# Performance work log

Measured on AMD Instinct MI355X. Metric: run time of the kernel, lower is better.

## Reference

```python
import jax, jax.numpy as jnp
import numpy as np

D_MODEL = 1024
NUM_HEADS = 16
D_K = D_MODEL // NUM_HEADS
SCALE = D_K ** 0.5


def setup_inputs() -> dict:
    key = jax.random.key(0)
    ks = jax.random.split(key, 11)
    B, S = 2, 2048
    std = 1.0 / np.sqrt(D_MODEL)
    inp = {
        "query": jax.random.normal(ks[0], (B, S, D_MODEL), dtype=jnp.float32),
        "key": jax.random.normal(ks[1], (B, S, D_MODEL), dtype=jnp.float32),
        "value": jax.random.normal(ks[2], (B, S, D_MODEL), dtype=jnp.float32),
        "wq": jax.random.uniform(ks[3], (D_MODEL, D_MODEL), jnp.float32, -std, std),
        "bq": jax.random.uniform(ks[4], (D_MODEL,), jnp.float32, -std, std),
        "wk": jax.random.uniform(ks[5], (D_MODEL, D_MODEL), jnp.float32, -std, std),
        "bk": jax.random.uniform(ks[6], (D_MODEL,), jnp.float32, -std, std),
        "wv": jax.random.uniform(ks[7], (D_MODEL, D_MODEL), jnp.float32, -std, std),
        "bv": jax.random.uniform(ks[8], (D_MODEL,), jnp.float32, -std, std),
        "wo": jax.random.uniform(ks[9], (D_MODEL, D_MODEL), jnp.float32, -std, std),
        "bo": jax.random.uniform(ks[10], (D_MODEL,), jnp.float32, -std, std),
    }
    return inp


def _split_heads(x):
    # [B, S, d_model] -> [B, H, S, d_k]
    B, S, _ = x.shape
    return x.reshape(B, S, NUM_HEADS, D_K).transpose(0, 2, 1, 3)


def reference(query, key, value, wq, bq, wk, bk, wv, bv, wo, bo):
    # Linear layers: torch Linear computes x @ W^T + b; weights here stored as [out, in]
    q = _split_heads(query @ wq.T + bq)  # [B, H, S, d_k]
    k = _split_heads(key @ wk.T + bk)
    v = _split_heads(value @ wv.T + bv)
    scores = jnp.einsum("bhqd,bhkd->bhqk", q, k) / SCALE  # [B, H, Sq, Sk]
    attn = jax.nn.softmax(scores, axis=-1)
    ctx = jnp.einsum("bhqk,bhkd->bhqd", attn, v)  # [B, H, S, d_k]
    B, H, S, dk = ctx.shape
    ctx = ctx.transpose(0, 2, 1, 3).reshape(B, S, D_MODEL)
    return ctx @ wo.T + bo
```

## Files before the change

kernel.cpp:

```cpp
#include <hip/hip_runtime.h>
#include <hip/hip_bf16.h>


typedef __attribute__((ext_vector_type(8))) short short8;
typedef __attribute__((ext_vector_type(4))) float floatx4;

#define D_MODEL 1024
#define SEQ 2048
#define NTOK 4096
#define DK 64
#define NH 16
#define MAT 4194304
#define WMAT 1048576

static __device__ __forceinline__ unsigned short f2bf(float f) {
    unsigned int x = __float_as_uint(f);
    unsigned int r = x + 0x7fffu + ((x >> 16) & 1u);
    return (unsigned short)(r >> 16);
}
static __device__ __forceinline__ float bf2f(unsigned short u) {
    return __uint_as_float(((unsigned int)u) << 16);
}
static __device__ __forceinline__ unsigned pk2(float x, float y) {
    __hip_bfloat162 h = __float22bfloat162_rn(make_float2(x, y));
    return *reinterpret_cast<unsigned*>(&h);
}
static __device__ __forceinline__ short8 cvt8(float4 f0, float4 f1) {
    union { unsigned u[4]; short8 s; } r;
    r.u[0] = pk2(f0.x, f0.y); r.u[1] = pk2(f0.z, f0.w);
    r.u[2] = pk2(f1.x, f1.y); r.u[3] = pk2(f1.z, f1.w);
    return r.s;
}

__global__ __launch_bounds__(256) void cvt7(
    const float* __restrict__ s0, const float* __restrict__ s1,
    const float* __restrict__ s2, const float* __restrict__ s3,
    const float* __restrict__ s4, const float* __restrict__ s5,
    const float* __restrict__ s6, unsigned short* __restrict__ dst) {
    const float* s; size_t doff; int n;
    switch (blockIdx.y) {
        case 0: s = s0; doff = 0;                          n = MAT;  break;
        case 1: s = s1; doff = (size_t)MAT;                n = MAT;  break;
        case 2: s = s2; doff = (size_t)2 * MAT;            n = MAT;  break;
        case 3: s = s3; doff = (size_t)3 * MAT;            n = WMAT; break;
        case 4: s = s4; doff = (size_t)3 * MAT + WMAT;     n = WMAT; break;
        case 5: s = s5; doff = (size_t)3 * MAT + 2 * WMAT; n = WMAT; break;
        default: s = s6; doff = (size_t)3 * MAT + 3 * WMAT; n = WMAT; break;
    }
    int idx = (blockIdx.x * 256 + threadIdx.x) * 8;
    if (idx >= n) return;
    float4 a = *(const float4*)(s + idx);
    float4 b = *(const float4*)(s + idx + 4);
    *(short8*)&dst[doff + idx] = cvt8(a, b);
}

template <bool F32OUT, bool ROWBIAS, int OSTRIDE>
static __device__ __forceinline__ void gemm_bb(const unsigned short* __restrict__ X,
                                               const unsigned short* __restrict__ W,
                                               const float* __restrict__ bias,
                                               void* __restrict__ outp) {
    __shared__ __align__(16) unsigned short Asm[128 * 72];
    __shared__ __align__(16) unsigned short Bsm[128 * 72];

    const int tid = threadIdx.x;
    const int lane = tid & 63;
    const int wv = tid >> 6;
    const int g = lane >> 4;
    const int lm = lane & 15;
    const int wr = wv >> 1;
    const int wc = wv & 1;
    const int m0 = blockIdx.y * 128;
    const int n0 = blockIdx.x * 128;

    floatx4 acc[4][4];
#pragma unroll
    for (int mi = 0; mi < 4; ++mi)
#pragma unroll
        for (int ni = 0; ni < 4; ++ni)
            acc[mi][ni] = (floatx4){0.f, 0.f, 0.f, 0.f};

    for (int k0 = 0; k0 < 1024; k0 += 64) {
#pragma unroll
        for (int i = 0; i < 4; ++i) {
            int idx = tid + i * 256;
            int row = idx >> 3;
            int col = (idx & 7) << 3;
            *(uint4*)&Asm[row * 72 + col] =
                *(const uint4*)&X[(size_t)(m0 + row) * 1024 + k0 + col];
            *(uint4*)&Bsm[row * 72 + col] =
                *(const uint4*)&W[(size_t)(n0 + row) * 1024 + k0 + col];
        }
        __syncthreads();
#pragma unroll
        for (int ks = 0; ks < 64; ks += 32) {
            short8 af[4], bfr[4];
#pragma unroll
            for (int mi = 0; mi < 4; ++mi)
                af[mi] = *(const short8*)&Asm[(wr * 64 + mi * 16 + lm) * 72 + ks + g * 8];
#pragma unroll
            for (int ni = 0; ni < 4; ++ni)
                bfr[ni] = *(const short8*)&Bsm[(wc * 64 + ni * 16 + lm) * 72 + ks + g * 8];
#pragma unroll
            for (int mi = 0; mi < 4; ++mi)
#pragma unroll
                for (int ni = 0; ni < 4; ++ni)
                    acc[mi][ni] = __builtin_amdgcn_mfma_f32_16x16x32_bf16(
                        af[mi], bfr[ni], acc[mi][ni], 0, 0, 0);
        }
        __syncthreads();
    }

    float cb[4];
#pragma unroll
    for (int ni = 0; ni < 4; ++ni)
        cb[ni] = ROWBIAS ? 0.f : bias[n0 + wc * 64 + ni * 16 + lm];
#pragma unroll
    for (int mi = 0; mi < 4; ++mi)
#pragma unroll
        for (int r = 0; r < 4; ++r) {
            int rowg = m0 + wr * 64 + mi * 16 + g * 4 + r;
            float rb = ROWBIAS ? bias[rowg] : 0.f;
#pragma unroll
            for (int ni = 0; ni < 4; ++ni) {
                int colg = n0 + wc * 64 + ni * 16 + lm;
                float val = acc[mi][ni][r] + (ROWBIAS ? rb : cb[ni]);
                if (F32OUT)
                    ((float*)outp)[(size_t)rowg * OSTRIDE + colg] = val;
                else
                    ((unsigned short*)outp)[(size_t)rowg * OSTRIDE + colg] = f2bf(val);
            }
        }
}

__global__ __launch_bounds__(256) void qkv_gemm_b(
    const unsigned short* __restrict__ Xb, const unsigned short* __restrict__ Wb,
    const float* __restrict__ bq, const float* __restrict__ bk,
    unsigned short* __restrict__ QK) {
    const int z = blockIdx.z;
    const float* bias = (z == 0) ? bq : bk;
    gemm_bb<false, false, 1024>(Xb + (size_t)z * MAT, Wb + (size_t)z * WMAT, bias,
                                QK + (size_t)z * MAT);
}

__global__ __launch_bounds__(256) void vt_gemm_b(
    const unsigned short* __restrict__ Wv, const unsigned short* __restrict__ Xv,
    const float* __restrict__ bv, unsigned short* __restrict__ VT) {
    gemm_bb<false, true, 4096>(Wv, Xv, bv, VT);
}

__global__ __launch_bounds__(256) void out_gemm_b(
    const unsigned short* __restrict__ ctx, const unsigned short* __restrict__ Wo,
    const float* __restrict__ bo, float* __restrict__ out) {
    gemm_bb<true, false, 1024>(ctx, Wo, bo, out);
}

template <bool ROWBIAS, int OSTRIDE>
static __device__ __forceinline__ void gemm128_f(const float* __restrict__ X,
                                                 const float* __restrict__ W,
                                                 const float* __restrict__ bias,
                                                 unsigned short* __restrict__ out) {
    __shared__ __align__(16) unsigned short Asm[128 * 72];
    __shared__ __align__(16) unsigned short Bsm[128 * 72];
    const int tid = threadIdx.x;
    const int lane = tid & 63;
    const int wv = tid >> 6;
    const int g = lane >> 4;
    const int lm = lane & 15;
    const int wr = wv >> 1;
    const int wc = wv & 1;
    const int m0 = blockIdx.y * 128;
    const int n0 = blockIdx.x * 128;
    floatx4 acc[4][4];
#pragma unroll
    for (int mi = 0; mi < 4; ++mi)
#pragma unroll
        for (int ni = 0; ni < 4; ++ni)
            acc[mi][ni] = (floatx4){0.f, 0.f, 0.f, 0.f};
    for (int k0 = 0; k0 < 1024; k0 += 64) {
#pragma unroll
        for (int i = 0; i < 4; ++i) {
            int idx = tid + i * 256;
            int row = idx >> 3;
            int col = (idx & 7) << 3;
            const float* sa = &X[(size_t)(m0 + row) * 1024 + k0 + col];
            *(short8*)&Asm[row * 72 + col] = cvt8(*(const float4*)sa, *(const float4*)(sa + 4));
            const float* sb = &W[(size_t)(n0 + row) * 1024 + k0 + col];
            *(short8*)&Bsm[row * 72 + col] = cvt8(*(const float4*)sb, *(const float4*)(sb + 4));
        }
        __syncthreads();
#pragma unroll
        for (int ks = 0; ks < 64; ks += 32) {
            short8 af[4], bfr[4];
#pragma unroll
            for (int mi = 0; mi < 4; ++mi)
                af[mi] = *(const short8*)&Asm[(wr * 64 + mi * 16 + lm) * 72 + ks + g * 8];
#pragma unroll
            for (int ni = 0; ni < 4; ++ni)
                bfr[ni] = *(const short8*)&Bsm[(wc * 64 + ni * 16 + lm) * 72 + ks + g * 8];
#pragma unroll
            for (int mi = 0; mi < 4; ++mi)
#pragma unroll
                for (int ni = 0; ni < 4; ++ni)
                    acc[mi][ni] = __builtin_amdgcn_mfma_f32_16x16x32_bf16(
                        af[mi], bfr[ni], acc[mi][ni], 0, 0, 0);
        }
        __syncthreads();
    }
    float cb[4];
#pragma unroll
    for (int ni = 0; ni < 4; ++ni)
        cb[ni] = ROWBIAS ? 0.f : bias[n0 + wc * 64 + ni * 16 + lm];
#pragma unroll
    for (int mi = 0; mi < 4; ++mi)
#pragma unroll
        for (int r = 0; r < 4; ++r) {
            int rowg = m0 + wr * 64 + mi * 16 + g * 4 + r;
            float rb = ROWBIAS ? bias[rowg] : 0.f;
#pragma unroll
            for (int ni = 0; ni < 4; ++ni) {
                int colg = n0 + wc * 64 + ni * 16 + lm;
                out[(size_t)rowg * OSTRIDE + colg] =
                    f2bf(acc[mi][ni][r] + (ROWBIAS ? rb : cb[ni]));
            }
        }
}

__global__ __launch_bounds__(256) void qkv_gemm_f(
    const float* __restrict__ xq, const float* __restrict__ xk,
    const float* __restrict__ wq, const float* __restrict__ wk,
    const float* __restrict__ bq, const float* __restrict__ bk,
    unsigned short* __restrict__ q, unsigned short* __restrict__ k) {
    if (blockIdx.z == 0) gemm128_f<false, 1024>(xq, wq, bq, q);
    else                 gemm128_f<false, 1024>(xk, wk, bk, k);
}

__global__ __launch_bounds__(256) void vt_gemm_f(
    const float* __restrict__ wv, const float* __restrict__ xv,
    const float* __restrict__ bv, unsigned short* __restrict__ VT) {
    gemm128_f<true, 4096>(wv, xv, bv, VT);
}

__global__ __launch_bounds__(256) void out_gemm_f(
    const float* __restrict__ wo, const float* __restrict__ bo,
    const unsigned short* __restrict__ ctx, float* __restrict__ out) {
    __shared__ __align__(16) unsigned short Asm[128 * 72];
    __shared__ __align__(16) unsigned short Bsm[128 * 72];
    const int tid = threadIdx.x;
    const int lane = tid & 63;
    const int wv = tid >> 6;
    const int g = lane >> 4;
    const int lm = lane & 15;
    const int wr = wv >> 1;
    const int wc = wv & 1;
    const int m0 = blockIdx.y * 128;
    const int n0 = blockIdx.x * 128;
    floatx4 acc[4][4];
#pragma unroll
    for (int mi = 0; mi < 4; ++mi)
#pragma unroll
        for (int ni = 0; ni < 4; ++ni)
            acc[mi][ni] = (floatx4){0.f, 0.f, 0.f, 0.f};
    for (int k0 = 0; k0 < 1024; k0 += 64) {
#pragma unroll
        for (int i = 0; i < 4; ++i) {
            int idx = tid + i * 256;
            int row = idx >> 3;
            int col = (idx & 7) << 3;
            *(uint4*)&Asm[row * 72 + col] =
                *(const uint4*)&ctx[(size_t)(m0 + row) * 1024 + k0 + col];
            const float* sb = &wo[(size_t)(n0 + row) * 1024 + k0 + col];
            *(short8*)&Bsm[row * 72 + col] = cvt8(*(const float4*)sb, *(const float4*)(sb + 4));
        }
        __syncthreads();
#pragma unroll
        for (int ks = 0; ks < 64; ks += 32) {
            short8 af[4], bfr[4];
#pragma unroll
            for (int mi = 0; mi < 4; ++mi)
                af[mi] = *(const short8*)&Asm[(wr * 64 + mi * 16 + lm) * 72 + ks + g * 8];
#pragma unroll
            for (int ni = 0; ni < 4; ++ni)
                bfr[ni] = *(const short8*)&Bsm[(wc * 64 + ni * 16 + lm) * 72 + ks + g * 8];
#pragma unroll
            for (int mi = 0; mi < 4; ++mi)
#pragma unroll
                for (int ni = 0; ni < 4; ++ni)
                    acc[mi][ni] = __builtin_amdgcn_mfma_f32_16x16x32_bf16(
                        af[mi], bfr[ni], acc[mi][ni], 0, 0, 0);
        }
        __syncthreads();
    }
    float bb[4];
#pragma unroll
    for (int ni = 0; ni < 4; ++ni)
        bb[ni] = bo[n0 + wc * 64 + ni * 16 + lm];
#pragma unroll
    for (int mi = 0; mi < 4; ++mi)
#pragma unroll
        for (int ni = 0; ni < 4; ++ni)
#pragma unroll
            for (int r = 0; r < 4; ++r) {
                int rowg = m0 + wr * 64 + mi * 16 + g * 4 + r;
                int colg = n0 + wc * 64 + ni * 16 + lm;
                out[(size_t)rowg * 1024 + colg] = acc[mi][ni][r] + bb[ni];
            }
}

__global__ __launch_bounds__(256) void attn_kernel(
    const unsigned short* __restrict__ Q, const unsigned short* __restrict__ K,
    const unsigned short* __restrict__ VT, unsigned short* __restrict__ CTX) {
    __shared__ __align__(16) unsigned short Ksm[64 * 72];
    __shared__ __align__(16) unsigned short Vt[64 * 72];

    const int tid = threadIdx.x;
    const int lane = tid & 63;
    const int w = tid >> 6;
    const int g = lane >> 4;
    const int lm = lane & 15;
    const int qt = blockIdx.x;
    const int bh = blockIdx.y;
    const int b = bh >> 4;
    const int h = bh & 15;

    const size_t base = (size_t)b * SEQ * D_MODEL + (size_t)h * DK;
    const size_t vtbase = (size_t)(h * 64) * NTOK + (size_t)b * SEQ;

    const int srow0 = tid >> 3;
    const int scol = (tid & 7) << 3;

    short8 qf[2];
    const int qrow = qt * 64 + w * 16 + lm;
#pragma unroll
    for (int t = 0; t < 2; ++t) {
        short8 raw = *(const short8*)&Q[base + (size_t)qrow * D_MODEL + t * 32 + g * 8];
        union { unsigned u[4]; short8 s; } r;
#pragma unroll
        for (int j = 0; j < 4; ++j) {
            float lo = bf2f((unsigned short)raw[2 * j]) * 0.125f;
            float hi = bf2f((unsigned short)raw[2 * j + 1]) * 0.125f;
            r.u[j] = pk2(lo, hi);
        }
        qf[t] = r.s;
    }

    float lsum = 0.f;
    floatx4 Oacc[4];
#pragma unroll
    for (int nb = 0; nb < 4; ++nb) Oacc[nb] = (floatx4){0.f, 0.f, 0.f, 0.f};

    for (int kt = 0; kt < SEQ / 64; ++kt) {
        const int krow0 = kt * 64;
#pragma unroll
        for (int i = 0; i < 2; ++i) {
            int row = srow0 + i * 32;
            *(uint4*)&Ksm[row * 72 + scol] =
                *(const uint4*)&K[base + (size_t)(krow0 + row) * D_MODEL + scol];
            *(uint4*)&Vt[row * 72 + scol] =
                *(const uint4*)&VT[vtbase + (size_t)row * NTOK + krow0 + scol];
        }
        __syncthreads();

        float p[4][4];
#pragma unroll
        for (int kb = 0; kb < 4; ++kb) {
            floatx4 a = (floatx4){0.f, 0.f, 0.f, 0.f};
#pragma unroll
            for (int t = 0; t < 2; ++t) {
                short8 ak = *(const short8*)&Ksm[(kb * 16 + lm) * 72 + t * 32 + g * 8];
                a = __builtin_amdgcn_mfma_f32_16x16x32_bf16(ak, qf[t], a, 0, 0, 0);
            }
#pragma unroll
            for (int r = 0; r < 4; ++r) p[kb][r] = __expf(a[r]);
            lsum += (p[kb][0] + p[kb][1]) + (p[kb][2] + p[kb][3]);
        }

#pragma unroll
        for (int cp = 0; cp < 2; ++cp) {
            const int c0 = 2 * cp, c1 = 2 * cp + 1;
            union { unsigned u[4]; short8 s; } ap;
            ap.u[0] = pk2(p[c0][0], p[c0][1]);
            ap.u[1] = pk2(p[c0][2], p[c0][3]);
            ap.u[2] = pk2(p[c1][0], p[c1][1]);
            ap.u[3] = pk2(p[c1][2], p[c1][3]);
#pragma unroll
            for (int nb = 0; nb < 4; ++nb) {
                const int d = nb * 16 + lm;
                uint2 x0 = *(const uint2*)&Vt[d * 72 + c0 * 16 + g * 4];
                uint2 x1 = *(const uint2*)&Vt[d * 72 + c1 * 16 + g * 4];
                union { unsigned u[4]; short8 s; } bv;
                bv.u[0] = x0.x; bv.u[1] = x0.y; bv.u[2] = x1.x; bv.u[3] = x1.y;
                Oacc[nb] = __builtin_amdgcn_mfma_f32_16x16x32_bf16(
                    ap.s, bv.s, Oacc[nb], 0, 0, 0);
            }
        }
        __syncthreads();
    }

    lsum += __shfl_xor(lsum, 16, 64);
    lsum += __shfl_xor(lsum, 32, 64);
    float lr[4];
#pragma unroll
    for (int r = 0; r < 4; ++r)
        lr[r] = __shfl(lsum, g * 4 + r, 64);

#pragma unroll
    for (int nb = 0; nb < 4; ++nb) {
#pragma unroll
        for (int r = 0; r < 4; ++r) {
            float val = Oacc[nb][r] / lr[r];
            int srow = qt * 64 + w * 16 + g * 4 + r;
            CTX[base + (size_t)srow * D_MODEL + nb * 16 + lm] = f2bf(val);
        }
    }
}

extern "C" void kernel_launch(void* const* d_in, const int* in_sizes, int n_in,
                              void* d_out, int out_size, void* d_ws, size_t ws_size,
                              hipStream_t stream) {
    const float* xq = (const float*)d_in[0];
    const float* xk = (const float*)d_in[1];
    const float* xv = (const float*)d_in[2];
    const float* wq = (const float*)d_in[3];
    const float* bq = (const float*)d_in[4];
    const float* wk = (const float*)d_in[5];
    const float* bk = (const float*)d_in[6];
    const float* wv = (const float*)d_in[7];
    const float* bv = (const float*)d_in[8];
    const float* wo = (const float*)d_in[9];
    const float* bo = (const float*)d_in[10];
    float* out = (float*)d_out;

    unsigned short* ws = (unsigned short*)d_ws;

    if (ws_size >= (size_t)68 * 1024 * 1024) {
        unsigned short* Xb = ws;
        unsigned short* Wb = ws + (size_t)3 * MAT;
        unsigned short* Qw = Wb + (size_t)4 * WMAT;
        unsigned short* Kw = Qw + (size_t)MAT;
        unsigned short* VTw = Kw + (size_t)MAT;
        unsigned short* Cw = VTw + (size_t)MAT;

        cvt7<<<dim3(2048, 7), 256, 0, stream>>>(xq, xk, xv, wq, wk, wv, wo, ws);
        qkv_gemm_b<<<dim3(8, 32, 2), 256, 0, stream>>>(Xb, Wb, bq, bk, Qw);
        vt_gemm_b<<<dim3(32, 8), 256, 0, stream>>>(
            Wb + (size_t)2 * WMAT, Xb + (size_t)2 * MAT, bv, VTw);
        attn_kernel<<<dim3(SEQ / 64, 2 * NH), 256, 0, stream>>>(Qw, Kw, VTw, Cw);
        out_gemm_b<<<dim3(8, 32), 256, 0, stream>>>(Cw, Wb + (size_t)3 * WMAT, bo, out);
    } else {
        unsigned short* Qw = ws;
        unsigned short* Kw = ws + (size_t)MAT;
        unsigned short* VTw = ws + (size_t)2 * MAT;
        unsigned short* Cw = ws + (size_t)3 * MAT;
        qkv_gemm_f<<<dim3(8, 32, 2), 256, 0, stream>>>(xq, xk, wq, wk, bq, bk, Qw, Kw);
        vt_gemm_f<<<dim3(32, 8), 256, 0, stream>>>(wv, xv, bv, VTw);
        attn_kernel<<<dim3(SEQ / 64, 2 * NH), 256, 0, stream>>>(Qw, Kw, VTw, Cw);
        out_gemm_f<<<dim3(8, 32), 256, 0, stream>>>(wo, bo, Cw, out);
    }
}
```

Measured before the change: 266.9 us.

## Swizzle LDS tiles, permute V^T token layout, double query rows per attention block

Replaces the padded 72-stride shared-memory tiles with XOR-swizzled 64-stride tiles in the GEMMs and attention to cut LDS bank conflicts. The V-transpose GEMM now writes tokens in a permuted order so the attention PV step can load each B fragment with a single 16-byte read instead of two 8-byte reads. Each attention block now processes 128 query rows (two 16-row slabs per wave), reusing each loaded K/V tile twice, and the grid is reordered so heads vary fastest. This raises register pressure and halves the number of attention blocks, which may reduce occupancy.

```diff
diff --git a/kernel.cpp b/kernel.cpp
--- a/kernel.cpp
+++ b/kernel.cpp
@@ -30,6 +30,9 @@
     r.u[0] = pk2(f0.x, f0.y); r.u[1] = pk2(f0.z, f0.w);
     r.u[2] = pk2(f1.x, f1.y); r.u[3] = pk2(f1.z, f1.w);
     return r.s;
+}
+static __device__ __forceinline__ int permtok(int t) {
+    return ((t >> 2) & 3) * 16 + ((t >> 4) & 3) * 4 + (t & 3);
 }
 
 __global__ __launch_bounds__(256) void cvt7(
@@ -54,13 +57,13 @@
     *(short8*)&dst[doff + idx] = cvt8(a, b);
 }
 
-template <bool F32OUT, bool ROWBIAS, int OSTRIDE>
+template <bool F32OUT, bool ROWBIAS, bool PERMN, int OSTRIDE>
 static __device__ __forceinline__ void gemm_bb(const unsigned short* __restrict__ X,
                                                const unsigned short* __restrict__ W,
                                                const float* __restrict__ bias,
                                                void* __restrict__ outp) {
-    __shared__ __align__(16) unsigned short Asm[128 * 72];
-    __shared__ __align__(16) unsigned short Bsm[128 * 72];
+    __shared__ __align__(16) unsigned short Asm[128 * 64];
+    __shared__ __align__(16) unsigned short Bsm[128 * 64];
 
     const int tid = threadIdx.x;
     const int lane = tid & 63;
@@ -71,6 +74,7 @@
     const int wc = wv & 1;
     const int m0 = blockIdx.y * 128;
     const int n0 = blockIdx.x * 128;
+    const int rs = (lm & 7) << 3;
 
     floatx4 acc[4][4];
 #pragma unroll
@@ -85,9 +89,10 @@
             int idx = tid + i * 256;
             int row = idx >> 3;
             int col = (idx & 7) << 3;
-            *(uint4*)&Asm[row * 72 + col] =
+            int sc = col ^ ((row & 7) << 3);
+            *(uint4*)&Asm[row * 64 + sc] =
                 *(const uint4*)&X[(size_t)(m0 + row) * 1024 + k0 + col];
-            *(uint4*)&Bsm[row * 72 + col] =
+            *(uint4*)&Bsm[row * 64 + sc] =
                 *(const uint4*)&W[(size_t)(n0 + row) * 1024 + k0 + col];
         }
         __syncthreads();
@@ -96,10 +101,12 @@
             short8 af[4], bfr[4];
 #pragma unroll
             for (int mi = 0; mi < 4; ++mi)
-                af[mi] = *(const short8*)&Asm[(wr * 64 + mi * 16 + lm) * 72 + ks + g * 8];
+                af[mi] = *(const short8*)&Asm[(wr * 64 + mi * 16 + lm) * 64 +
+                                              ((ks + g * 8) ^ rs)];
 #pragma unroll
             for (int ni = 0; ni < 4; ++ni)
-                bfr[ni] = *(const short8*)&Bsm[(wc * 64 + ni * 16 + lm) * 72 + ks + g * 8];
+                bfr[ni] = *(const short8*)&Bsm[(wc * 64 + ni * 16 + lm) * 64 +
+                                               ((ks + g * 8) ^ rs)];
 #pragma unroll
             for (int mi = 0; mi < 4; ++mi)
 #pragma unroll
@@ -123,6 +130,7 @@
 #pragma unroll
             for (int ni = 0; ni < 4; ++ni) {
                 int colg = n0 + wc * 64 + ni * 16 + lm;
+                if (PERMN) colg = (colg & ~63) | permtok(colg & 63);
                 float val = acc[mi][ni][r] + (ROWBIAS ? rb : cb[ni]);
                 if (F32OUT)
                     ((float*)outp)[(size_t)rowg * OSTRIDE + colg] = val;
@@ -138,23 +146,23 @@
     unsigned short* __restrict__ QK) {
     const int z = blockIdx.z;
     const float* bias = (z == 0) ? bq : bk;
-    gemm_bb<false, false, 1024>(Xb + (size_t)z * MAT, Wb + (size_t)z * WMAT, bias,
-                                QK + (size_t)z * MAT);
+    gemm_bb<false, false, false, 1024>(Xb + (size_t)z * MAT, Wb + (size_t)z * WMAT,
+                                       bias, QK + (size_t)z * MAT);
 }
 
 __global__ __launch_bounds__(256) void vt_gemm_b(
     const unsigned short* __restrict__ Wv, const unsigned short* __restrict__ Xv,
     const float* __restrict__ bv, unsigned short* __restrict__ VT) {
-    gemm_bb<false, true, 4096>(Wv, Xv, bv, VT);
+    gemm_bb<false, true, true, 4096>(Wv, Xv, bv, VT);
 }
 
 __global__ __launch_bounds__(256) void out_gemm_b(
     const unsigned short* __restrict__ ctx, const unsigned short* __restrict__ Wo,
     const float* __restrict__ bo, float* __restrict__ out) {
-    gemm_bb<true, false, 1024>(ctx, Wo, bo, out);
-}
-
-template <bool ROWBIAS, int OSTRIDE>
+    gemm_bb<true, false, false, 1024>(ctx, Wo, bo, out);
+}
+
+template <bool ROWBIAS, bool PERMN, int OSTRIDE>
 static __device__ __forceinline__ void gemm128_f(const float* __restrict__ X,
                                                  const float* __restrict__ W,
                                                  const float* __restrict__ bias,
@@ -219,6 +227,7 @@
 #pragma unroll
             for (int ni = 0; ni < 4; ++ni) {
                 int colg = n0 + wc * 64 + ni * 16 + lm;
+                if (PERMN) colg = (colg & ~63) | permtok(colg & 63);
                 out[(size_t)rowg * OSTRIDE + colg] =
                     f2bf(acc[mi][ni][r] + (ROWBIAS ? rb : cb[ni]));
             }
@@ -230,14 +239,14 @@
     const float* __restrict__ wq, const float* __restrict__ wk,
     const float* __restrict__ bq, const float* __restrict__ bk,
     unsigned short* __restrict__ q, unsigned short* __restrict__ k) {
-    if (blockIdx.z == 0) gemm128_f<false, 1024>(xq, wq, bq, q);
-    else                 gemm128_f<false, 1024>(xk, wk, bk, k);
+    if (blockIdx.z == 0) gemm128_f<false, false, 1024>(xq, wq, bq, q);
+    else                 gemm128_f<false, false, 1024>(xk, wk, bk, k);
 }
 
 __global__ __launch_bounds__(256) void vt_gemm_f(
     const float* __restrict__ wv, const float* __restrict__ xv,
     const float* __restrict__ bv, unsigned short* __restrict__ VT) {
-    gemm128_f<true, 4096>(wv, xv, bv, VT);
+    gemm128_f<true, true, 4096>(wv, xv, bv, VT);
 }
 
 __global__ __launch_bounds__(256) void out_gemm_f(
@@ -309,16 +318,16 @@
 __global__ __launch_bounds__(256) void attn_kernel(
     const unsigned short* __restrict__ Q, const unsigned short* __restrict__ K,
     const unsigned short* __restrict__ VT, unsigned short* __restrict__ CTX) {
-    __shared__ __align__(16) unsigned short Ksm[64 * 72];
-    __shared__ __align__(16) unsigned short Vt[64 * 72];
+    __shared__ __align__(16) unsigned short Ksm[64 * 64];
+    __shared__ __align__(16) unsigned short Vt[64 * 64];
 
     const int tid = threadIdx.x;
     const int lane = tid & 63;
     const int w = tid >> 6;
     const int g = lane >> 4;
     const int lm = lane & 15;
-    const int qt = blockIdx.x;
-    const int bh = blockIdx.y;
+    const int bh = blockIdx.x;
+    const int qt = blockIdx.y;
     const int b = bh >> 4;
     const int h = bh & 15;
 
@@ -327,89 +336,103 @@
 
     const int srow0 = tid >> 3;
     const int scol = (tid & 7) << 3;
-
-    short8 qf[2];
-    const int qrow = qt * 64 + w * 16 + lm;
-#pragma unroll
-    for (int t = 0; t < 2; ++t) {
-        short8 raw = *(const short8*)&Q[base + (size_t)qrow * D_MODEL + t * 32 + g * 8];
-        union { unsigned u[4]; short8 s; } r;
-#pragma unroll
-        for (int j = 0; j < 4; ++j) {
-            float lo = bf2f((unsigned short)raw[2 * j]) * 0.125f;
-            float hi = bf2f((unsigned short)raw[2 * j + 1]) * 0.125f;
-            r.u[j] = pk2(lo, hi);
-        }
-        qf[t] = r.s;
-    }
-
-    float lsum = 0.f;
-    floatx4 Oacc[4];
-#pragma unroll
-    for (int nb = 0; nb < 4; ++nb) Oacc[nb] = (floatx4){0.f, 0.f, 0.f, 0.f};
+    const int swz = scol ^ ((srow0 & 7) << 3);
+    const int rs = (lm & 7) << 3;
+
+    short8 qf[2][2];
+#pragma unroll
+    for (int qs = 0; qs < 2; ++qs) {
+        const int qrow = qt * 128 + w * 32 + qs * 16 + lm;
+#pragma unroll
+        for (int t = 0; t < 2; ++t) {
+            short8 raw = *(const short8*)&Q[base + (size_t)qrow * D_MODEL + t * 32 + g * 8];
+            union { unsigned u[4]; short8 s; } r;
+#pragma unroll
+            for (int j = 0; j < 4; ++j) {
+                float lo = bf2f((unsigned short)raw[2 * j]) * 0.125f;
+                float hi = bf2f((unsigned short)raw[2 * j + 1]) * 0.125f;
+                r.u[j] = pk2(lo, hi);
+            }
+            qf[qs][t] = r.s;
+        }
+    }
+
+    float lsum[2] = {0.f, 0.f};
+    floatx4 Oacc[2][4];
+#pragma unroll
+    for (int qs = 0; qs < 2; ++qs)
+#pragma unroll
+        for (int nb = 0; nb < 4; ++nb) Oacc[qs][nb] = (floatx4){0.f, 0.f, 0.f, 0.f};
 
     for (int kt = 0; kt < SEQ / 64; ++kt) {
         const int krow0 = kt * 64;
 #pragma unroll
         for (int i = 0; i < 2; ++i) {
             int row = srow0 + i * 32;
-            *(uint4*)&Ksm[row * 72 + scol] =
+            *(uint4*)&Ksm[row * 64 + swz] =
                 *(const uint4*)&K[base + (size_t)(krow0 + row) * D_MODEL + scol];
-            *(uint4*)&Vt[row * 72 + scol] =
+            *(uint4*)&Vt[row * 64 + swz] =
                 *(const uint4*)&VT[vtbase + (size_t)row * NTOK + krow0 + scol];
         }
         __syncthreads();
 
-        float p[4][4];
+        float p[2][4][4];
 #pragma unroll
         for (int kb = 0; kb < 4; ++kb) {
-            floatx4 a = (floatx4){0.f, 0.f, 0.f, 0.f};
-#pragma unroll
-            for (int t = 0; t < 2; ++t) {
-                short8 ak = *(const short8*)&Ksm[(kb * 16 + lm) * 72 + t * 32 + g * 8];
-                a = __builtin_amdgcn_mfma_f32_16x16x32_bf16(ak, qf[t], a, 0, 0, 0);
-            }
-#pragma unroll
-            for (int r = 0; r < 4; ++r) p[kb][r] = __expf(a[r]);
-            lsum += (p[kb][0] + p[kb][1]) + (p[kb][2] + p[kb][3]);
+            short8 ak0 = *(const short8*)&Ksm[(kb * 16 + lm) * 64 + ((0 + g * 8) ^ rs)];
+            short8 ak1 = *(const short8*)&Ksm[(kb * 16 + lm) * 64 + ((32 + g * 8) ^ rs)];
+#pragma unroll
+            for (int qs = 0; qs < 2; ++qs) {
+                floatx4 a = (floatx4){0.f, 0.f, 0.f, 0.f};
+                a = __builtin_amdgcn_mfma_f32_16x16x32_bf16(ak0, qf[qs][0], a, 0, 0, 0);
+                a = __builtin_amdgcn_mfma_f32_16x16x32_bf16(ak1, qf[qs][1], a, 0, 0, 0);
+#pragma unroll
+                for (int r = 0; r < 4; ++r) p[qs][kb][r] = __expf(a[r]);
+                lsum[qs] += (p[qs][kb][0] + p[qs][kb][1]) + (p[qs][kb][2] + p[qs][kb][3]);
+            }
         }
 
 #pragma unroll
         for (int cp = 0; cp < 2; ++cp) {
             const int c0 = 2 * cp, c1 = 2 * cp + 1;
-            union { unsigned u[4]; short8 s; } ap;
-            ap.u[0] = pk2(p[c0][0], p[c0][1]);
-            ap.u[1] = pk2(p[c0][2], p[c0][3]);
-            ap.u[2] = pk2(p[c1][0], p[c1][1]);
-            ap.u[3] = pk2(p[c1][2], p[c1][3]);
+            union { unsigned u[4]; short8 s; } ap[2];
+#pragma unroll
+            for (int qs = 0; qs < 2; ++qs) {
+                ap[qs].u[0] = pk2(p[qs][c0][0], p[qs][c0][1]);
+                ap[qs].u[1] = pk2(p[qs][c0][2], p[qs][c0][3]);
+                ap[qs].u[2] = pk2(p[qs][c1][0], p[qs][c1][1]);
+                ap[qs].u[3] = pk2(p[qs][c1][2], p[qs][c1][3]);
+            }
 #pragma unroll
             for (int nb = 0; nb < 4; ++nb) {
                 const int d = nb * 16 + lm;
-                uint2 x0 = *(const uint2*)&Vt[d * 72 + c0 * 16 + g * 4];
-                uint2 x1 = *(const uint2*)&Vt[d * 72 + c1 * 16 + g * 4];
-                union { unsigned u[4]; short8 s; } bv;
-                bv.u[0] = x0.x; bv.u[1] = x0.y; bv.u[2] = x1.x; bv.u[3] = x1.y;
-                Oacc[nb] = __builtin_amdgcn_mfma_f32_16x16x32_bf16(
-                    ap.s, bv.s, Oacc[nb], 0, 0, 0);
-            }
-        }
-        __syncthreads();
-    }
-
-    lsum += __shfl_xor(lsum, 16, 64);
-    lsum += __shfl_xor(lsum, 32, 64);
-    float lr[4];
-#pragma unroll
-    for (int r = 0; r < 4; ++r)
-        lr[r] = __shfl(lsum, g * 4 + r, 64);
-
-#pragma unroll
-    for (int nb = 0; nb < 4; ++nb) {
-#pragma unroll
-        for (int r = 0; r < 4; ++r) {
-            float val = Oacc[nb][r] / lr[r];
-            int srow = qt * 64 + w * 16 + g * 4 + r;
-            CTX[base + (size_t)srow * D_MODEL + nb * 16 + lm] = f2bf(val);
+                short8 bv = *(const short8*)&Vt[d * 64 + ((g * 16 + cp * 8) ^ rs)];
+                Oacc[0][nb] = __builtin_amdgcn_mfma_f32_16x16x32_bf16(
+                    ap[0].s, bv, Oacc[0][nb], 0, 0, 0);
+                Oacc[1][nb] = __builtin_amdgcn_mfma_f32_16x16x32_bf16(
+                    ap[1].s, bv, Oacc[1][nb], 0, 0, 0);
+            }
+        }
+        __syncthreads();
+    }
+
+#pragma unroll
+    for (int qs = 0; qs < 2; ++qs) {
+        float l = lsum[qs];
+        l += __shfl_xor(l, 16, 64);
+        l += __shfl_xor(l, 32, 64);
+        float lr[4];
+#pragma unroll
+        for (int r = 0; r < 4; ++r)
+            lr[r] = __shfl(l, g * 4 + r, 64);
+#pragma unroll
+        for (int nb = 0; nb < 4; ++nb) {
+#pragma unroll
+            for (int r = 0; r < 4; ++r) {
+                float val = Oacc[qs][nb][r] / lr[r];
+                int srow = qt * 128 + w * 32 + qs * 16 + g * 4 + r;
+                CTX[base + (size_t)srow * D_MODEL + nb * 16 + lm] = f2bf(val);
+            }
         }
     }
 }
@@ -444,7 +467,7 @@
         qkv_gemm_b<<<dim3(8, 32, 2), 256, 0, stream>>>(Xb, Wb, bq, bk, Qw);
         vt_gemm_b<<<dim3(32, 8), 256, 0, stream>>>(
             Wb + (size_t)2 * WMAT, Xb + (size_t)2 * MAT, bv, VTw);
-        attn_kernel<<<dim3(SEQ / 64, 2 * NH), 256, 0, stream>>>(Qw, Kw, VTw, Cw);
+        attn_kernel<<<dim3(2 * NH, SEQ / 128), 256, 0, stream>>>(Qw, Kw, VTw, Cw);
         out_gemm_b<<<dim3(8, 32), 256, 0, stream>>>(Cw, Wb + (size_t)3 * WMAT, bo, out);
     } else {
         unsigned short* Qw = ws;
@@ -453,7 +476,7 @@
         unsigned short* Cw = ws + (size_t)3 * MAT;
         qkv_gemm_f<<<dim3(8, 32, 2), 256, 0, stream>>>(xq, xk, wq, wk, bq, bk, Qw, Kw);
         vt_gemm_f<<<dim3(32, 8), 256, 0, stream>>>(wv, xv, bv, VTw);
-        attn_kernel<<<dim3(SEQ / 64, 2 * NH), 256, 0, stream>>>(Qw, Kw, VTw, Cw);
+        attn_kernel<<<dim3(2 * NH, SEQ / 128), 256, 0, stream>>>(Qw, Kw, VTw, Cw);
         out_gemm_f<<<dim3(8, 32), 256, 0, stream>>>(wo, bo, Cw, out);
     }
 }
```

Measured after the change: 246.0 us. 1.09x faster.
